# Kernel tuning notes

Measured on AMD Instinct MI355X. Metric: run time of the kernel, lower is better.

## Reference

```python
import jax, jax.numpy as jnp
import numpy as np


def setup_inputs() -> dict:
    key = jax.random.key(0)
    k1, k2, k3 = jax.random.split(key, 3)
    x = jax.random.normal(k1, (16, 2048, 4096), dtype=jnp.float32)
    # learned parameters: degrees (5,4) -> 6 numerator coeffs, 4 denominator coeffs
    center = jnp.zeros((1,), dtype=jnp.float32)
    numerator = jax.random.normal(k2, (6,), dtype=jnp.float32) * 0.5
    denominator = jax.random.normal(k3, (4,), dtype=jnp.float32) * 0.5
    return {"x": x, "center": center, "numerator": numerator, "denominator": denominator}


def reference(x, center, numerator, denominator):
    # PAU version A: out = P(z) / Q(z), z = x + center
    #   P(z) = a0 + a1 z + ... + a5 z^5           (Horner)
    #   Q(z) = 1 + |b1 z| + |b2 z^2| + ... + |b4 z^4|
    #        = 1 + |z| * (|b1| + |z|*(|b2| + |z|*(|b3| + |z|*|b4|)))
    z = x + center[0]
    # numerator via Horner's scheme
    p = numerator[-1]
    for i in range(numerator.shape[0] - 2, -1, -1):
        p = p * z + numerator[i]
    # denominator via Horner's scheme on |z| with |b_j|
    az = jnp.abs(z)
    q = jnp.abs(denominator[-1])
    for i in range(denominator.shape[0] - 2, -1, -1):
        q = q * az + jnp.abs(denominator[i])
    q = q * az + 1.0
    return p / q
```

## Files before the change

kernel.cpp:

```cpp
#include <hip/hip_runtime.h>


__global__ __launch_bounds__(256) void PAU_kernel(
    const float* __restrict__ x,
    const float* __restrict__ center,
    const float* __restrict__ num,
    const float* __restrict__ den,
    float* __restrict__ out,
    long long n4,
    long long n)
{
    const float c  = center[0];
    const float a0 = num[0], a1 = num[1], a2 = num[2],
                a3 = num[3], a4 = num[4], a5 = num[5];
    const float b1 = fabsf(den[0]), b2 = fabsf(den[1]),
                b3 = fabsf(den[2]), b4 = fabsf(den[3]);

    const long long i = (long long)blockIdx.x * blockDim.x + threadIdx.x;

    if (i < n4) {
        float4 v = reinterpret_cast<const float4*>(x)[i];
        float4 r;
        float* vp = &v.x;
        float* rp = &r.x;
#pragma unroll
        for (int k = 0; k < 4; ++k) {
            const float z = vp[k] + c;
            float p = fmaf(a5, z, a4);
            p = fmaf(p, z, a3);
            p = fmaf(p, z, a2);
            p = fmaf(p, z, a1);
            p = fmaf(p, z, a0);
            const float az = fabsf(z);
            float q = fmaf(b4, az, b3);
            q = fmaf(q, az, b2);
            q = fmaf(q, az, b1);
            q = fmaf(q, az, 1.0f);
            rp[k] = p / q;
        }
        reinterpret_cast<float4*>(out)[i] = r;
    }

    if (i == 0) {
        for (long long t = n4 * 4; t < n; ++t) {
            const float z = x[t] + c;
            float p = fmaf(a5, z, a4);
            p = fmaf(p, z, a3);
            p = fmaf(p, z, a2);
            p = fmaf(p, z, a1);
            p = fmaf(p, z, a0);
            const float az = fabsf(z);
            float q = fmaf(b4, az, b3);
            q = fmaf(q, az, b2);
            q = fmaf(q, az, b1);
            q = fmaf(q, az, 1.0f);
            out[t] = p / q;
        }
    }
}

extern "C" void kernel_launch(void* const* d_in, const int* in_sizes, int n_in,
                              void* d_out, int out_size, void* d_ws, size_t ws_size,
                              hipStream_t stream) {
    const float* x      = (const float*)d_in[0];
    const float* center = (const float*)d_in[1];
    const float* num    = (const float*)d_in[2];
    const float* den    = (const float*)d_in[3];
    float* out          = (float*)d_out;

    const long long n  = (long long)in_sizes[0];
    const long long n4 = n / 4;

    const int block = 256;
    const long long grid = (n4 + block - 1) / block;

    PAU_kernel<<<(unsigned)grid, block, 0, stream>>>(x, center, num, den, out, n4, n);
}
```

Baseline: 809.5 us.

## Use grid-stride loop with nontemporal vector I/O and fast reciprocal

Replaces the one-thread-per-float4 launch with a capped grid of 2048 blocks and a grid-stride loop that issues four independent float4 loads per iteration. Loads and stores use nontemporal builtins so the streamed data bypasses cache retention, and the IEEE division is replaced with multiplication by the hardware reciprocal. The aim is more memory-level parallelism and less division cost in a bandwidth-bound elementwise kernel. The fast reciprocal slightly reduces accuracy, and the capped grid may under-occupy the device.

```diff
diff --git a/kernel.cpp b/kernel.cpp
--- a/kernel.cpp
+++ b/kernel.cpp
@@ -1,5 +1,39 @@
 #include <hip/hip_runtime.h>
 
+
+typedef float floatx4 __attribute__((ext_vector_type(4)));
+
+__device__ __forceinline__ float pau_eval(
+    float xv, float c,
+    float a0, float a1, float a2, float a3, float a4, float a5,
+    float b1, float b2, float b3, float b4)
+{
+    const float z = xv + c;
+    float p = fmaf(a5, z, a4);
+    p = fmaf(p, z, a3);
+    p = fmaf(p, z, a2);
+    p = fmaf(p, z, a1);
+    p = fmaf(p, z, a0);
+    const float az = fabsf(z);
+    float q = fmaf(b4, az, b3);
+    q = fmaf(q, az, b2);
+    q = fmaf(q, az, b1);
+    q = fmaf(q, az, 1.0f);
+    return p * __builtin_amdgcn_rcpf(q);
+}
+
+__device__ __forceinline__ floatx4 pau_eval4(
+    floatx4 v, float c,
+    float a0, float a1, float a2, float a3, float a4, float a5,
+    float b1, float b2, float b3, float b4)
+{
+    floatx4 r;
+    r.x = pau_eval(v.x, c, a0,a1,a2,a3,a4,a5, b1,b2,b3,b4);
+    r.y = pau_eval(v.y, c, a0,a1,a2,a3,a4,a5, b1,b2,b3,b4);
+    r.z = pau_eval(v.z, c, a0,a1,a2,a3,a4,a5, b1,b2,b3,b4);
+    r.w = pau_eval(v.w, c, a0,a1,a2,a3,a4,a5, b1,b2,b3,b4);
+    return r;
+}
 
 __global__ __launch_bounds__(256) void PAU_kernel(
     const float* __restrict__ x,
@@ -16,45 +50,38 @@
     const float b1 = fabsf(den[0]), b2 = fabsf(den[1]),
                 b3 = fabsf(den[2]), b4 = fabsf(den[3]);
 
-    const long long i = (long long)blockIdx.x * blockDim.x + threadIdx.x;
+    const long long S = (long long)gridDim.x * blockDim.x;
+    long long i = (long long)blockIdx.x * blockDim.x + threadIdx.x;
 
-    if (i < n4) {
-        float4 v = reinterpret_cast<const float4*>(x)[i];
-        float4 r;
-        float* vp = &v.x;
-        float* rp = &r.x;
-#pragma unroll
-        for (int k = 0; k < 4; ++k) {
-            const float z = vp[k] + c;
-            float p = fmaf(a5, z, a4);
-            p = fmaf(p, z, a3);
-            p = fmaf(p, z, a2);
-            p = fmaf(p, z, a1);
-            p = fmaf(p, z, a0);
-            const float az = fabsf(z);
-            float q = fmaf(b4, az, b3);
-            q = fmaf(q, az, b2);
-            q = fmaf(q, az, b1);
-            q = fmaf(q, az, 1.0f);
-            rp[k] = p / q;
-        }
-        reinterpret_cast<float4*>(out)[i] = r;
+    const floatx4* __restrict__ xin  = reinterpret_cast<const floatx4*>(x);
+    floatx4* __restrict__       yout = reinterpret_cast<floatx4*>(out);
+
+    for (; i + 3 * S < n4; i += 4 * S) {
+        floatx4 v0 = __builtin_nontemporal_load(xin + i);
+        floatx4 v1 = __builtin_nontemporal_load(xin + i + S);
+        floatx4 v2 = __builtin_nontemporal_load(xin + i + 2 * S);
+        floatx4 v3 = __builtin_nontemporal_load(xin + i + 3 * S);
+
+        floatx4 r0 = pau_eval4(v0, c, a0,a1,a2,a3,a4,a5, b1,b2,b3,b4);
+        floatx4 r1 = pau_eval4(v1, c, a0,a1,a2,a3,a4,a5, b1,b2,b3,b4);
+        floatx4 r2 = pau_eval4(v2, c, a0,a1,a2,a3,a4,a5, b1,b2,b3,b4);
+        floatx4 r3 = pau_eval4(v3, c, a0,a1,a2,a3,a4,a5, b1,b2,b3,b4);
+
+        __builtin_nontemporal_store(r0, yout + i);
+        __builtin_nontemporal_store(r1, yout + i + S);
+        __builtin_nontemporal_store(r2, yout + i + 2 * S);
+        __builtin_nontemporal_store(r3, yout + i + 3 * S);
     }
 
-    if (i == 0) {
+    for (; i < n4; i += S) {
+        floatx4 v = __builtin_nontemporal_load(xin + i);
+        floatx4 r = pau_eval4(v, c, a0,a1,a2,a3,a4,a5, b1,b2,b3,b4);
+        __builtin_nontemporal_store(r, yout + i);
+    }
+
+    if (blockIdx.x == 0 && threadIdx.x == 0) {
         for (long long t = n4 * 4; t < n; ++t) {
-            const float z = x[t] + c;
-            float p = fmaf(a5, z, a4);
-            p = fmaf(p, z, a3);
-            p = fmaf(p, z, a2);
-            p = fmaf(p, z, a1);
-            p = fmaf(p, z, a0);
-            const float az = fabsf(z);
-            float q = fmaf(b4, az, b3);
-            q = fmaf(q, az, b2);
-            q = fmaf(q, az, b1);
-            q = fmaf(q, az, 1.0f);
-            out[t] = p / q;
+            out[t] = pau_eval(x[t], c, a0,a1,a2,a3,a4,a5, b1,b2,b3,b4);
         }
     }
 }
@@ -72,7 +99,9 @@
     const long long n4 = n / 4;
 
     const int block = 256;
-    const long long grid = (n4 + block - 1) / block;
+    long long grid = (n4 + block - 1) / block;
+    if (grid > 2048) grid = 2048;
+    if (grid < 1) grid = 1;
 
     PAU_kernel<<<(unsigned)grid, block, 0, stream>>>(x, center, num, den, out, n4, n);
 }
```

Result: slower. 887.2 us (+9.6%).
